# Performance work log

Hardware: AMD Instinct MI355X
Metric: run time of the kernel (lower is better)

The kernel has to match this reference:

```python
import jax, jax.numpy as jnp
import numpy as np

B, L, C, H = 4, 2048, 1024, 16
D = C // H            # head_dim = 64
TAU = 4
SCALE = 1.0 / np.sqrt(D) / TAU  # cos_attn=False path


def setup_inputs() -> dict:
    key = jax.random.key(0)
    ks = jax.random.split(key, 7)
    std = 1.0 / np.sqrt(C)
    return {
        "x": jax.random.normal(ks[0], (B, L, C), dtype=jnp.float32),
        "attn_bias": jax.random.normal(ks[1], (1, 1, L, L), dtype=jnp.float32) * 0.02,
        "W_qkv": jax.random.normal(ks[2], (3 * C, C), dtype=jnp.float32) * std,
        "q_bias": jax.random.normal(ks[3], (C,), dtype=jnp.float32) * 0.02,
        "v_bias": jax.random.normal(ks[4], (C,), dtype=jnp.float32) * 0.02,
        "W_proj": jax.random.normal(ks[5], (C, C), dtype=jnp.float32) * std,
        "b_proj": jax.random.normal(ks[6], (C,), dtype=jnp.float32) * 0.02,
    }


def reference(x, attn_bias, W_qkv, q_bias, v_bias, W_proj, b_proj):
    # qkv projection with bias = cat(q_bias, zeros_k, v_bias)
    bias = jnp.concatenate([q_bias, jnp.zeros_like(q_bias), v_bias])
    qkv = x @ W_qkv.T + bias                      # [B, L, 3C]
    qkv = qkv.reshape(B, L, 3, H, D)
    q, k, v = jnp.moveaxis(qkv, 2, 0)             # each [B, L, H, D]
    q = q.transpose(0, 2, 1, 3)                   # [B, H, L, D]
    k = k.transpose(0, 2, 1, 3)
    v = v.transpose(0, 2, 1, 3)
    # slow_attn: (q*scale) @ k^T + bias -> softmax -> @ v
    scores = jnp.einsum("bhqd,bhkd->bhqk", q * SCALE, k) + attn_bias
    attn = jax.nn.softmax(scores, axis=-1)
    oup = jnp.einsum("bhqk,bhkd->bhqd", attn, v)  # [B, H, L, D]
    oup = oup.transpose(0, 2, 1, 3).reshape(B, L, C)
    return oup @ W_proj.T + b_proj
```

## Files before the change

kernel.cpp:

```cpp
#include <hip/hip_runtime.h>
#include <hip/hip_bf16.h>

typedef unsigned short u16;
typedef unsigned int   u32;

using f32x4  = __attribute__((ext_vector_type(4)))  float;
using f32x16 = __attribute__((ext_vector_type(16))) float;
using s16x8  = __attribute__((ext_vector_type(8)))  short;
using b16x8  = __attribute__((ext_vector_type(8)))  __bf16;
using u32x4  = __attribute__((ext_vector_type(4)))  u32;

#define LOG2E 1.44269504088896f
#define QSC   (0.03125f * LOG2E)

__device__ __forceinline__ f32x4 mfma16(s16x8 a, s16x8 b, f32x4 c) {
  return __builtin_amdgcn_mfma_f32_16x16x32_bf16(
      __builtin_bit_cast(b16x8, a), __builtin_bit_cast(b16x8, b), c, 0, 0, 0);
}
__device__ __forceinline__ f32x16 mfma32(s16x8 a, s16x8 b, f32x16 c) {
  return __builtin_amdgcn_mfma_f32_32x32x16_bf16(
      __builtin_bit_cast(b16x8, a), __builtin_bit_cast(b16x8, b), c, 0, 0, 0);
}

__device__ __forceinline__ u16 f2bf(float f) {
  u32 u = __builtin_bit_cast(u32, f);
  u = (u + 0x7FFFu + ((u >> 16) & 1u)) >> 16;
  return (u16)u;
}
__device__ __forceinline__ float exp2_hw(float x) {
  float r;
  asm("v_exp_f32 %0, %1" : "=v"(r) : "v"(x));
  return r;
}
__device__ __forceinline__ u32 cvtpk(float a, float b) {
  u32 r;
  asm("v_cvt_pk_bf16_f32 %0, %1, %2" : "=v"(r) : "v"(a), "v"(b));
  return r;
}

__device__ __forceinline__ void gload16(const void* g, void* l) {
  __builtin_amdgcn_global_load_lds(
      (const __attribute__((address_space(1))) u32*)g,
      (__attribute__((address_space(3))) u32*)l, 16, 0, 0);
}

__global__ void cvt(const float* __restrict__ in, u16* __restrict__ out, int n4) {
  int i = blockIdx.x * blockDim.x + threadIdx.x;
  int stride = gridDim.x * blockDim.x;
  for (; i < n4; i += stride) {
    float4 v = ((const float4*)in)[i];
    ushort4 o;
    o.x = f2bf(v.x); o.y = f2bf(v.y); o.z = f2bf(v.z); o.w = f2bf(v.w);
    ((ushort4*)out)[i] = o;
  }
}

__global__ void bias_rearrange(const float* __restrict__ ab, u16* __restrict__ out) {
  const int idx  = blockIdx.x * 256 + threadIdx.x;
  const int lane = idx & 63;
  const int vo   = ((idx >> 6) & 3) * 8;
  const int kt   = (idx >> 8) & 31;
  const int slot = idx >> 13;
  const int hi   = lane >> 5;
  const int q    = slot * 32 + (lane & 31);
  const int kb   = vo >> 4;
  const int so   = (vo & 8) << 1;
  const int kbase = kt * 64 + kb * 32 + so + 4 * hi;
  const float* src = ab + (long)q * 2048 + kbase;
  const float4 a = *(const float4*)(src);
  const float4 b = *(const float4*)(src + 8);
  u16 o[8];
  o[0] = f2bf(a.x * LOG2E); o[1] = f2bf(a.y * LOG2E);
  o[2] = f2bf(a.z * LOG2E); o[3] = f2bf(a.w * LOG2E);
  o[4] = f2bf(b.x * LOG2E); o[5] = f2bf(b.y * LOG2E);
  o[6] = f2bf(b.z * LOG2E); o[7] = f2bf(b.w * LOG2E);
  *(s16x8*)(out + (long)idx * 8) = *(s16x8*)o;
}

template<int EPI>
__global__ __launch_bounds__(256)
void gemm_bt(const u16* __restrict__ A, const u16* __restrict__ Bm,
             int M, int N, int K,
             const float* __restrict__ bias0, const float* __restrict__ bias1,
             u16* __restrict__ oq, u16* __restrict__ ok, u16* __restrict__ ov,
             float* __restrict__ outf)
{
  __shared__ u16 As[2][128 * 32];
  __shared__ u16 Bs[2][128 * 32];

  const int tid  = threadIdx.x;
  const int w    = tid >> 6;
  const int lane = tid & 63;
  const int lr   = lane & 15;
  const int lg   = lane >> 4;
  const int wr   = w >> 1, wc = w & 1;

  const int bm = blockIdx.y, bn = blockIdx.x;

  f32x4 acc[4][4];
#pragma unroll
  for (int i = 0; i < 4; ++i)
#pragma unroll
    for (int j = 0; j < 4; ++j) acc[i][j] = (f32x4){0.f, 0.f, 0.f, 0.f};

  const int rowA = bm * 128 + (tid >> 2);
  const int rowB = bn * 128 + (tid >> 2);
  const int colk = (tid & 3) * 8;

  const u16* ga0 = A  + (long)rowA * K + colk;
  const u16* gb0 = Bm + (long)rowB * K + colk;

  gload16(ga0,          &As[0][w * 512]);
  gload16(ga0 + 64 * K, &As[0][2048 + w * 512]);
  gload16(gb0,          &Bs[0][w * 512]);
  gload16(gb0 + 64 * K, &Bs[0][2048 + w * 512]);
  asm volatile("s_waitcnt vmcnt(0)" ::: "memory");
  __syncthreads();

  const int NT = K >> 5;
  for (int t = 0; t < NT; ++t) {
    const int cur = t & 1;
    if (t + 1 < NT) {
      const u16* ga = ga0 + (t + 1) * 32;
      const u16* gb = gb0 + (t + 1) * 32;
      gload16(ga,          &As[cur ^ 1][w * 512]);
      gload16(ga + 64 * K, &As[cur ^ 1][2048 + w * 512]);
      gload16(gb,          &Bs[cur ^ 1][w * 512]);
      gload16(gb + 64 * K, &Bs[cur ^ 1][2048 + w * 512]);
    }

    s16x8 af[4], bfr[4];
#pragma unroll
    for (int mi = 0; mi < 4; ++mi)
      af[mi] = *(const s16x8*)(&As[cur][(wr * 64 + mi * 16 + lr) * 32 + lg * 8]);
#pragma unroll
    for (int ni = 0; ni < 4; ++ni)
      bfr[ni] = *(const s16x8*)(&Bs[cur][(wc * 64 + ni * 16 + lr) * 32 + lg * 8]);
#pragma unroll
    for (int mi = 0; mi < 4; ++mi)
#pragma unroll
      for (int ni = 0; ni < 4; ++ni)
        acc[mi][ni] = mfma16(af[mi], bfr[ni], acc[mi][ni]);

    asm volatile("s_waitcnt vmcnt(0)" ::: "memory");
    __syncthreads();
  }

  const int gm0 = bm * 128 + wr * 64;
  const int gn0 = bn * 128 + wc * 64;

#pragma unroll
  for (int mi = 0; mi < 4; ++mi) {
#pragma unroll
    for (int ni = 0; ni < 4; ++ni) {
      const int col  = gn0 + ni * 16 + lr;
      const int row0 = gm0 + mi * 16 + lg * 4;
      if (EPI == 0) {
        const int which = col >> 10;
        const int cj    = col & 1023;
        const float badd = (which == 0) ? bias0[cj] : (which == 2 ? bias1[cj] : 0.f);
        const int h = cj >> 6, d = cj & 63;
#pragma unroll
        for (int r = 0; r < 4; ++r) {
          const int rowg = row0 + r;
          const int b = rowg >> 11, l = rowg & 2047;
          const int bh = b * 16 + h;
          float val = acc[mi][ni][r] + badd;
          if (which == 0) val *= QSC;
          const u16 o = f2bf(val);
          if (which == 0)      oq[(bh * 2048 + l) * 64 + d] = o;
          else if (which == 1) ok[(bh * 2048 + l) * 64 + d] = o;
          else {
            const int lp = (l & ~12) | ((l & 4) << 1) | ((l & 8) >> 1);
            ov[(bh * 64 + d) * 2048 + lp] = o;
          }
        }
      } else {
        const float badd = bias0[col];
#pragma unroll
        for (int r = 0; r < 4; ++r)
          outf[(long)(row0 + r) * N + col] = acc[mi][ni][r] + badd;
      }
    }
  }
}

__global__ __launch_bounds__(256)
void flash_attn(const u16* __restrict__ qbuf, const u16* __restrict__ kbuf,
                const u16* __restrict__ vtbuf, const u16* __restrict__ biasr,
                u16* __restrict__ oup)
{
  __shared__ u16 Ks[2][64 * 72];
  __shared__ u16 Vs[2][64 * 72];

  const int tid  = threadIdx.x;
  const int w    = tid >> 6;
  const int lane = tid & 63;
  const int lq   = lane & 31;
  const int hi   = lane >> 5;

  const int bid = blockIdx.x;
  const int swz = (bid & 7) * 128 + (bid >> 3);
  const int bh  = swz >> 4, qt2 = swz & 15;
  const long base = (long)bh * (2048 * 64);

  const int qrow = qt2 * 128 + w * 32 + lq;
  s16x8 qf[4];
  {
    const u16* qp = qbuf + base + qrow * 64 + 8 * hi;
#pragma unroll
    for (int s = 0; s < 4; ++s) qf[s] = *(const s16x8*)(qp + 16 * s);
  }

  f32x16 oacc0, oacc1;
  float lacc[8];
#pragma unroll
  for (int r = 0; r < 16; ++r) { oacc0[r] = 0.f; oacc1[r] = 0.f; }
#pragma unroll
  for (int r = 0; r < 8; ++r) lacc[r] = 0.f;

  const u16* bslice = biasr + (long)(qt2 * 4 + w) * 65536 + lane * 8;

  const int sr  = tid >> 3;
  const int scc = tid & 7;
  const u16* kg = kbuf  + base + sr * 64   + scc * 8;
  const u16* vg = vtbuf + base + sr * 2048 + scc * 8;
  const int wo0 = sr * 72 + scc * 8;
  const int wo1 = (32 + sr) * 72 + scc * 8;

  {
    const s16x8 a0 = *(const s16x8*)(kg);
    const s16x8 a1 = *(const s16x8*)(kg + 2048);
    const s16x8 b0 = *(const s16x8*)(vg);
    const s16x8 b1 = *(const s16x8*)(vg + 65536);
    *(s16x8*)(&Ks[0][wo0]) = a0;  *(s16x8*)(&Ks[0][wo1]) = a1;
    *(s16x8*)(&Vs[0][wo0]) = b0;  *(s16x8*)(&Vs[0][wo1]) = b1;
  }
  __syncthreads();

  for (int kt = 0; kt < 32; ++kt) {
    const int cur = kt & 1;

    s16x8 nk0, nk1, nv0, nv1;
    if (kt < 31) {
      const u16* kn = kg + (kt + 1) * 4096;
      const u16* vn = vg + (kt + 1) * 64;
      nk0 = *(const s16x8*)(kn);
      nk1 = *(const s16x8*)(kn + 2048);
      nv0 = *(const s16x8*)(vn);
      nv1 = *(const s16x8*)(vn + 65536);
    }

    s16x8 kf0[4], kf1[4], vf0[4], vf1[4];
    {
      const u16* kb0 = &Ks[cur][lq * 72];
      const u16* kb1 = &Ks[cur][(32 + lq) * 72];
      const u16* vb0 = &Vs[cur][lq * 72];
      const u16* vb1 = &Vs[cur][(32 + lq) * 72];
#pragma unroll
      for (int s = 0; s < 4; ++s) {
        const int off = (2 * s + hi) * 8;
        kf0[s] = *(const s16x8*)(kb0 + off);
        kf1[s] = *(const s16x8*)(kb1 + off);
        vf0[s] = *(const s16x8*)(vb0 + off);
        vf1[s] = *(const s16x8*)(vb1 + off);
      }
    }

    u32x4 bb[4];
#pragma unroll
    for (int k = 0; k < 4; ++k)
      bb[k] = *(const u32x4*)(bslice + kt * 2048 + k * 512);

    f32x16 sa0, sa1;
#pragma unroll
    for (int jw = 0; jw < 8; ++jw) {
      const u32 w0 = bb[jw >> 2][jw & 3];
      const u32 w1 = bb[2 + (jw >> 2)][jw & 3];
      sa0[2 * jw]     = __builtin_bit_cast(float, w0 << 16);
      sa0[2 * jw + 1] = __builtin_bit_cast(float, w0 & 0xFFFF0000u);
      sa1[2 * jw]     = __builtin_bit_cast(float, w1 << 16);
      sa1[2 * jw + 1] = __builtin_bit_cast(float, w1 & 0xFFFF0000u);
    }

#pragma unroll
    for (int s = 0; s < 4; ++s) sa0 = mfma32(kf0[s], qf[s], sa0);
#pragma unroll
    for (int s = 0; s < 4; ++s) sa1 = mfma32(kf1[s], qf[s], sa1);

#pragma unroll
    for (int r = 0; r < 16; ++r) {
      sa0[r] = exp2_hw(sa0[r]);
      sa1[r] = exp2_hw(sa1[r]);
    }
#pragma unroll
    for (int r = 0; r < 8; ++r)
      lacc[r] += (sa0[r] + sa0[r + 8]) + (sa1[r] + sa1[r + 8]);

    s16x8 pf[4];
#pragma unroll
    for (int ks = 0; ks < 4; ++ks) {
      const f32x16 ps = (ks & 2) ? sa1 : sa0;
      const int o = (ks & 1) * 8;
      u32x4 tt;
      tt[0] = cvtpk(ps[o + 0], ps[o + 1]);
      tt[1] = cvtpk(ps[o + 2], ps[o + 3]);
      tt[2] = cvtpk(ps[o + 4], ps[o + 5]);
      tt[3] = cvtpk(ps[o + 6], ps[o + 7]);
      pf[ks] = __builtin_bit_cast(s16x8, tt);
    }

#pragma unroll
    for (int ks = 0; ks < 4; ++ks) {
      oacc0 = mfma32(vf0[ks], pf[ks], oacc0);
      oacc1 = mfma32(vf1[ks], pf[ks], oacc1);
    }

    if (kt < 31) {
      *(s16x8*)(&Ks[cur ^ 1][wo0]) = nk0;
      *(s16x8*)(&Ks[cur ^ 1][wo1]) = nk1;
      *(s16x8*)(&Vs[cur ^ 1][wo0]) = nv0;
      *(s16x8*)(&Vs[cur ^ 1][wo1]) = nv1;
    }
    __syncthreads();
  }

  u32 (*Os)[32][33] = (u32(*)[32][33])&Ks[0][0];
  const int b = bh >> 4, h = bh & 15;
  float l = ((lacc[0] + lacc[1]) + (lacc[2] + lacc[3]))
          + ((lacc[4] + lacc[5]) + (lacc[6] + lacc[7]));
  l += __shfl_xor(l, 32, 64);
  const float inv = 1.f / l;
#pragma unroll
  for (int i = 0; i < 8; ++i) {
    const int idx = (i & 1) + 2 * hi + 4 * (i >> 1);
    Os[w][lq][idx]      = cvtpk(oacc0[2 * i] * inv, oacc0[2 * i + 1] * inv);
    Os[w][lq][idx + 16] = cvtpk(oacc1[2 * i] * inv, oacc1[2 * i + 1] * inv);
  }
  __syncthreads();
#pragma unroll
  for (int it = 0; it < 4; ++it) {
    const int q = it * 8 + (lane >> 3);
    const int c = (lane & 7) * 4;
    u32x4 v;
#pragma unroll
    for (int j = 0; j < 4; ++j) v[j] = Os[w][q][c + j];
    const long row = (long)(b * 2048 + qt2 * 128 + w * 32 + q);
    *(u32x4*)(oup + row * 1024 + h * 64 + (lane & 7) * 8) = v;
  }
}

extern "C" void kernel_launch(void* const* d_in, const int* in_sizes, int n_in,
                              void* d_out, int out_size, void* d_ws, size_t ws_size,
                              hipStream_t stream) {
  const float* x     = (const float*)d_in[0];
  const float* ab    = (const float*)d_in[1];
  const float* wqkv  = (const float*)d_in[2];
  const float* qbias = (const float*)d_in[3];
  const float* vbias = (const float*)d_in[4];
  const float* wproj = (const float*)d_in[5];
  const float* bproj = (const float*)d_in[6];
  float* out = (float*)d_out;

  char* ws = (char*)d_ws;
  if (ws_size < 83886080u) return;
  u16* xb     = (u16*)(ws);
  u16* wqkvb  = (u16*)(ws + 16777216);
  u16* wprojb = (u16*)(ws + 23068672);
  u16* biasr  = (u16*)(ws + 25165824);
  u16* qbuf   = (u16*)(ws + 33554432);
  u16* kbuf   = (u16*)(ws + 50331648);
  u16* vtbuf  = (u16*)(ws + 67108864);

  cvt<<<dim3(2048), dim3(256), 0, stream>>>(x, xb, 8388608 / 4);
  cvt<<<dim3(512),  dim3(256), 0, stream>>>(wqkv, wqkvb, 3145728 / 4);
  cvt<<<dim3(256),  dim3(256), 0, stream>>>(wproj, wprojb, 1048576 / 4);
  bias_rearrange<<<dim3(2048), dim3(256), 0, stream>>>(ab, biasr);

  gemm_bt<0><<<dim3(24, 64), dim3(256), 0, stream>>>(
      xb, wqkvb, 8192, 3072, 1024, qbias, vbias, qbuf, kbuf, vtbuf, nullptr);

  flash_attn<<<dim3(1024), dim3(256), 0, stream>>>(qbuf, kbuf, vtbuf, biasr, xb);

  gemm_bt<1><<<dim3(8, 64), dim3(256), 0, stream>>>(
      xb, wprojb, 8192, 1024, 1024, bproj, nullptr, nullptr, nullptr, nullptr, out);
}
```

Measured before the change: 234.7 us.

## Merge conversion kernels, coalesce bias rearrange via LDS, prioritize MFMA waves

Replaces three fp32-to-bf16 conversion launches with one kernel covering x, W_qkv and W_proj, which works because their bf16 outputs are contiguous in the workspace. Rewrites the attention-bias rearrangement to read coalesced rows into shared memory and permute from there, instead of doing strided global reads. Adds s_setprio around the MFMA blocks in flash attention so waves issuing matrix ops get scheduling priority. This trims launch overhead and uncoalesced traffic, at the cost of an extra LDS round trip and barrier in the bias kernel.

```diff
diff --git a/kernel.cpp b/kernel.cpp
--- a/kernel.cpp
+++ b/kernel.cpp
@@ -44,11 +44,15 @@
       (__attribute__((address_space(3))) u32*)l, 16, 0, 0);
 }
 
-__global__ void cvt(const float* __restrict__ in, u16* __restrict__ out, int n4) {
+__global__ void cvt3(const float* __restrict__ x, const float* __restrict__ wqkv,
+                     const float* __restrict__ wproj, u16* __restrict__ out) {
   int i = blockIdx.x * blockDim.x + threadIdx.x;
-  int stride = gridDim.x * blockDim.x;
-  for (; i < n4; i += stride) {
-    float4 v = ((const float4*)in)[i];
+  const int stride = gridDim.x * blockDim.x;
+  for (; i < 3145728; i += stride) {
+    const float* src = (i < 2097152) ? x + 4 * (long)i
+                     : (i < 2883584) ? wqkv + 4 * ((long)i - 2097152)
+                                     : wproj + 4 * ((long)i - 2883584);
+    const float4 v = *(const float4*)src;
     ushort4 o;
     o.x = f2bf(v.x); o.y = f2bf(v.y); o.z = f2bf(v.z); o.w = f2bf(v.w);
     ((ushort4*)out)[i] = o;
@@ -56,25 +60,41 @@
 }
 
 __global__ void bias_rearrange(const float* __restrict__ ab, u16* __restrict__ out) {
-  const int idx  = blockIdx.x * 256 + threadIdx.x;
-  const int lane = idx & 63;
-  const int vo   = ((idx >> 6) & 3) * 8;
-  const int kt   = (idx >> 8) & 31;
-  const int slot = idx >> 13;
-  const int hi   = lane >> 5;
-  const int q    = slot * 32 + (lane & 31);
-  const int kb   = vo >> 4;
-  const int so   = (vo & 8) << 1;
-  const int kbase = kt * 64 + kb * 32 + so + 4 * hi;
-  const float* src = ab + (long)q * 2048 + kbase;
-  const float4 a = *(const float4*)(src);
-  const float4 b = *(const float4*)(src + 8);
-  u16 o[8];
-  o[0] = f2bf(a.x * LOG2E); o[1] = f2bf(a.y * LOG2E);
-  o[2] = f2bf(a.z * LOG2E); o[3] = f2bf(a.w * LOG2E);
-  o[4] = f2bf(b.x * LOG2E); o[5] = f2bf(b.y * LOG2E);
-  o[6] = f2bf(b.z * LOG2E); o[7] = f2bf(b.w * LOG2E);
-  *(s16x8*)(out + (long)idx * 8) = *(s16x8*)o;
+  __shared__ u16 T[32][72];
+  const int tid  = threadIdx.x;
+  const int slot = blockIdx.x >> 5;
+  const int kt   = blockIdx.x & 31;
+
+  {
+    const int qr = tid >> 3;
+    const int fc = (tid & 7) * 8;
+    const float* src = ab + (long)(slot * 32 + qr) * 2048 + kt * 64 + fc;
+    const float4 a = *(const float4*)(src);
+    const float4 b = *(const float4*)(src + 4);
+    u16 t[8];
+    t[0] = f2bf(a.x * LOG2E); t[1] = f2bf(a.y * LOG2E);
+    t[2] = f2bf(a.z * LOG2E); t[3] = f2bf(a.w * LOG2E);
+    t[4] = f2bf(b.x * LOG2E); t[5] = f2bf(b.y * LOG2E);
+    t[6] = f2bf(b.z * LOG2E); t[7] = f2bf(b.w * LOG2E);
+    *(s16x8*)&T[qr][fc] = *(s16x8*)t;
+  }
+  __syncthreads();
+
+  {
+    const int chunk = tid >> 6;
+    const int lane  = tid & 63;
+    const int q5    = lane & 31;
+    const int hi    = lane >> 5;
+    u16 o[8];
+#pragma unroll
+    for (int e = 0; e < 8; ++e) {
+      const int vidx = chunk * 8 + e;
+      const int kb = vidx >> 4, r = vidx & 15;
+      const int key = kb * 32 + (r & 3) + 8 * (r >> 2) + 4 * hi;
+      o[e] = T[q5][key];
+    }
+    *(s16x8*)(out + ((long)blockIdx.x * 256 + tid) * 8) = *(s16x8*)o;
+  }
 }
 
 template<int EPI>
@@ -283,10 +303,12 @@
       sa1[2 * jw + 1] = __builtin_bit_cast(float, w1 & 0xFFFF0000u);
     }
 
+    __builtin_amdgcn_s_setprio(1);
 #pragma unroll
     for (int s = 0; s < 4; ++s) sa0 = mfma32(kf0[s], qf[s], sa0);
 #pragma unroll
     for (int s = 0; s < 4; ++s) sa1 = mfma32(kf1[s], qf[s], sa1);
+    __builtin_amdgcn_s_setprio(0);
 
 #pragma unroll
     for (int r = 0; r < 16; ++r) {
@@ -310,11 +332,13 @@
       pf[ks] = __builtin_bit_cast(s16x8, tt);
     }
 
+    __builtin_amdgcn_s_setprio(1);
 #pragma unroll
     for (int ks = 0; ks < 4; ++ks) {
       oacc0 = mfma32(vf0[ks], pf[ks], oacc0);
       oacc1 = mfma32(vf1[ks], pf[ks], oacc1);
     }
+    __builtin_amdgcn_s_setprio(0);
 
     if (kt < 31) {
       *(s16x8*)(&Ks[cur ^ 1][wo0]) = nk0;
@@ -372,9 +396,7 @@
   u16* kbuf   = (u16*)(ws + 50331648);
   u16* vtbuf  = (u16*)(ws + 67108864);
 
-  cvt<<<dim3(2048), dim3(256), 0, stream>>>(x, xb, 8388608 / 4);
-  cvt<<<dim3(512),  dim3(256), 0, stream>>>(wqkv, wqkvb, 3145728 / 4);
-  cvt<<<dim3(256),  dim3(256), 0, stream>>>(wproj, wprojb, 1048576 / 4);
+  cvt3<<<dim3(2048), dim3(256), 0, stream>>>(x, wqkv, wproj, xb);
   bias_rearrange<<<dim3(2048), dim3(256), 0, stream>>>(ab, biasr);
 
   gemm_bt<0><<<dim3(24, 64), dim3(256), 0, stream>>>(
```

Result: no change. 239.2 us (+1.9%).
